# Kernel optimization log

Measured on AMD Instinct MI355X. Metric: run time of the kernel, lower is better.

Reference implementation:

```python
import jax, jax.numpy as jnp
import numpy as np

B = 64          # graphs per batch
MAX_NODES = 512 # nodes per graph
N = B * MAX_NODES
DEG = 16
E = N * DEG
F_IN = 12
H, D = 4, 32    # heads, per-head dim
HID = H * D     # 128
A = 512         # num_outputs (action space)
NEG_SLOPE = 0.2


def setup_inputs() -> dict:
    key = jax.random.key(0)
    ks = jax.random.split(key, 32)
    x = jax.random.normal(ks[0], (N, F_IN), dtype=jnp.float32)
    # edges confined within each graph's node block (as in the torch adjacency loop)
    src_l = jax.random.randint(ks[1], (B, MAX_NODES * DEG), 0, MAX_NODES, dtype=jnp.int32)
    dst_l = jax.random.randint(ks[2], (B, MAX_NODES * DEG), 0, MAX_NODES, dtype=jnp.int32)
    offs = (jnp.arange(B, dtype=jnp.int32) * MAX_NODES)[:, None]
    edge_src = (src_l + offs).reshape(-1)
    edge_dst = (dst_l + offs).reshape(-1)
    batch_idx = jnp.repeat(jnp.arange(B, dtype=jnp.int32), MAX_NODES)

    s = 0.1
    p = {}
    p["Wl0"] = s * jax.random.normal(ks[3], (F_IN, H, D), dtype=jnp.float32)
    p["Wr0"] = s * jax.random.normal(ks[4], (F_IN, H, D), dtype=jnp.float32)
    p["att0"] = s * jax.random.normal(ks[5], (H, D), dtype=jnp.float32)
    p["b0"] = jnp.zeros((HID,), dtype=jnp.float32)
    p["Wl"] = s * jax.random.normal(ks[6], (3, HID, H, D), dtype=jnp.float32)
    p["Wr"] = s * jax.random.normal(ks[7], (3, HID, H, D), dtype=jnp.float32)
    p["att"] = s * jax.random.normal(ks[8], (3, H, D), dtype=jnp.float32)
    p["b"] = jnp.zeros((3, HID), dtype=jnp.float32)
    p["qW1"] = s * jax.random.normal(ks[9], (2 * HID, HID), dtype=jnp.float32)
    p["qb1"] = jnp.zeros((HID,), dtype=jnp.float32)
    p["qW2"] = s * jax.random.normal(ks[10], (HID, A), dtype=jnp.float32)
    p["qb2"] = jnp.zeros((A,), dtype=jnp.float32)
    p["vW1"] = s * jax.random.normal(ks[11], (2 * HID, HID), dtype=jnp.float32)
    p["vb1"] = jnp.zeros((HID,), dtype=jnp.float32)
    p["vW2"] = s * jax.random.normal(ks[12], (HID, 1), dtype=jnp.float32)
    p["vb2"] = jnp.zeros((1,), dtype=jnp.float32)
    return dict(x=x, edge_src=edge_src, edge_dst=edge_dst, batch_idx=batch_idx, **p)


def _gatv2(x, src, dst, Wl, Wr, att, b):
    n = x.shape[0]
    xl = jnp.einsum('nf,fhd->nhd', x, Wl)  # source transform [N,H,D]
    xr = jnp.einsum('nf,fhd->nhd', x, Wr)  # target transform [N,H,D]
    xj = xl[src]                            # [E,H,D]
    e = jax.nn.leaky_relu(xj + xr[dst], NEG_SLOPE)
    s = jnp.einsum('ehd,hd->eh', e, att)    # [E,H]
    smax = jax.ops.segment_max(s, dst, num_segments=n)
    smax = jnp.where(jnp.isfinite(smax), smax, 0.0)
    a = jnp.exp(s - smax[dst])
    den = jax.ops.segment_sum(a, dst, num_segments=n)
    a = a / jnp.maximum(den[dst], 1e-16)
    out = jax.ops.segment_sum(a[:, :, None] * xj, dst, num_segments=n)  # [N,H,D]
    return out.reshape(n, H * D) + b


def reference(x, edge_src, edge_dst, batch_idx,
              Wl0, Wr0, att0, b0, Wl, Wr, att, b,
              qW1, qb1, qW2, qb2, vW1, vb1, vW2, vb2):
    h = jax.nn.relu(_gatv2(x, edge_src, edge_dst, Wl0, Wr0, att0, b0))
    for i in range(3):  # remaining num_layers-1 GATv2 layers (dropout off in eval)
        h = jax.nn.relu(_gatv2(h, edge_src, edge_dst, Wl[i], Wr[i], att[i], b[i]))
    nb = h.shape[0] // MAX_NODES
    gsum = jax.ops.segment_sum(h, batch_idx, num_segments=nb)
    cnt = jax.ops.segment_sum(jnp.ones((h.shape[0], 1), h.dtype), batch_idx, num_segments=nb)
    gmean = gsum / jnp.maximum(cnt, 1.0)
    gmax = jax.ops.segment_max(h, batch_idx, num_segments=nb)
    g = jnp.concatenate([gmean, gmax], axis=-1)  # [B, 2*HID]
    adv = jax.nn.relu(g @ qW1 + qb1) @ qW2 + qb2
    val = jax.nn.relu(g @ vW1 + vb1) @ vW2 + vb2
    q = val + (adv - adv.mean(axis=-1, keepdims=True))
    return q
```

## Files before the change

### kernel.cpp

```cpp
#include <hip/hip_runtime.h>
#include <hip/hip_bf16.h>

#define NN 32768
#define EE 524288
#define HID 128
#define BGRAPH 64
#define MAXN 512
#define AOUT 512
#define MAXDEG 64

typedef __attribute__((ext_vector_type(8))) short short8;
typedef __attribute__((ext_vector_type(4))) float f32x4;
typedef unsigned short ushort;
typedef unsigned int uint;

__device__ __forceinline__ ushort bf16_rn(float f) {
    uint u = __float_as_uint(f);
    u += 0x7FFF + ((u >> 16) & 1);
    return (ushort)(u >> 16);
}
__device__ __forceinline__ void bf16_split(float f, ushort& hi, ushort& lo) {
    hi = bf16_rn(f);
    float fh = __uint_as_float(((uint)hi) << 16);
    lo = bf16_rn(f - fh);
}

__device__ __forceinline__ float vsum4(f32x4 v) {
    return (v.x + v.y) + (v.z + v.w);
}

__global__ __launch_bounds__(256) void setup_kernel(
    const int* __restrict__ src, const int* __restrict__ dst,
    int* __restrict__ cursor, int* __restrict__ bucket,
    const float* __restrict__ Wl, const float* __restrict__ Wr,
    ushort* __restrict__ wt_hi, ushort* __restrict__ wt_lo) {
    int blk = blockIdx.x;
    if (blk < EE / 256) {
        int i = blk * 256 + threadIdx.x;
        int d = dst[i];
        int p = atomicAdd(&cursor[d], 1);
        if (p < MAXDEG) bucket[(size_t)d * MAXDEG + p] = src[i];
    } else {
        int idx = (blk - EE / 256) * 256 + threadIdx.x;
        if (idx >= 98304) return;
        int c = idx & 127;
        int k = (idx >> 7) & 127;
        int l = (idx >> 14) % 3;
        int lr = idx / 49152;
        float v = (lr ? Wr : Wl)[l * 16384 + k * 128 + c];
        ushort hi, lo;
        bf16_split(v, hi, lo);
        int ct = c >> 4, m = c & 15;
        int ks = k >> 5;
        int lane = (((k >> 3) & 3) << 4) | m;
        int j = k & 7;
        size_t o = ((size_t)(lr * 3 + l) * 32 + ct * 4 + ks) * 512 + lane * 8 + j;
        wt_hi[o] = hi;
        wt_lo[o] = lo;
    }
}

template<int KTOT, int KC>
__global__ __launch_bounds__(256) void transform3(
    const float* __restrict__ hin, const float* __restrict__ Wl,
    const float* __restrict__ Wr, float* __restrict__ xl, float* __restrict__ xr) {
    __shared__ float wb[KC][256];
    __shared__ float ha[KC][36];
    int b = blockIdx.x;
    int xcd = b & 7, slot = b >> 3;
    int graph = xcd + 8 * (slot >> 4);
    int chunk = slot & 15;
    int node0 = graph * 512 + chunk * 32;
    int t = threadIdx.x;
    int c32 = t & 31;
    int ng  = t >> 5;
    const float4* wl4g = (const float4*)Wl;
    const float4* wr4g = (const float4*)Wr;
    for (int idx = t; idx < KC * 64; idx += 256) {
        int k = idx >> 6, r = idx & 63;
        float4 v = (r < 32) ? wl4g[k * 32 + r] : wr4g[k * 32 + (r - 32)];
        ((float4*)&wb[k][0])[r] = v;
    }
    for (int idx = t; idx < 32 * KC; idx += 256) {
        int m = idx / KC, kk = idx - m * KC;
        ha[kk][m] = hin[(size_t)(node0 + m) * KTOT + kk];
    }
    __syncthreads();
    float4 accL[4], accR[4];
#pragma unroll
    for (int m = 0; m < 4; m++) {
        accL[m].x = accL[m].y = accL[m].z = accL[m].w = 0.f;
        accR[m].x = accR[m].y = accR[m].z = accR[m].w = 0.f;
    }
#pragma unroll
    for (int kk = 0; kk < KC; kk++) {
        float4 wl = ((const float4*)&wb[kk][0])[c32];
        float4 wr = ((const float4*)&wb[kk][128])[c32];
        float4 hv = *(const float4*)&ha[kk][ng * 4];
        accL[0].x = fmaf(hv.x, wl.x, accL[0].x); accL[0].y = fmaf(hv.x, wl.y, accL[0].y);
        accL[0].z = fmaf(hv.x, wl.z, accL[0].z); accL[0].w = fmaf(hv.x, wl.w, accL[0].w);
        accL[1].x = fmaf(hv.y, wl.x, accL[1].x); accL[1].y = fmaf(hv.y, wl.y, accL[1].y);
        accL[1].z = fmaf(hv.y, wl.z, accL[1].z); accL[1].w = fmaf(hv.y, wl.w, accL[1].w);
        accL[2].x = fmaf(hv.z, wl.x, accL[2].x); accL[2].y = fmaf(hv.z, wl.y, accL[2].y);
        accL[2].z = fmaf(hv.z, wl.z, accL[2].z); accL[2].w = fmaf(hv.z, wl.w, accL[2].w);
        accL[3].x = fmaf(hv.w, wl.x, accL[3].x); accL[3].y = fmaf(hv.w, wl.y, accL[3].y);
        accL[3].z = fmaf(hv.w, wl.z, accL[3].z); accL[3].w = fmaf(hv.w, wl.w, accL[3].w);
        accR[0].x = fmaf(hv.x, wr.x, accR[0].x); accR[0].y = fmaf(hv.x, wr.y, accR[0].y);
        accR[0].z = fmaf(hv.x, wr.z, accR[0].z); accR[0].w = fmaf(hv.x, wr.w, accR[0].w);
        accR[1].x = fmaf(hv.y, wr.x, accR[1].x); accR[1].y = fmaf(hv.y, wr.y, accR[1].y);
        accR[1].z = fmaf(hv.y, wr.z, accR[1].z); accR[1].w = fmaf(hv.y, wr.w, accR[1].w);
        accR[2].x = fmaf(hv.z, wr.x, accR[2].x); accR[2].y = fmaf(hv.z, wr.y, accR[2].y);
        accR[2].z = fmaf(hv.z, wr.z, accR[2].z); accR[2].w = fmaf(hv.z, wr.w, accR[2].w);
        accR[3].x = fmaf(hv.w, wr.x, accR[3].x); accR[3].y = fmaf(hv.w, wr.y, accR[3].y);
        accR[3].z = fmaf(hv.w, wr.z, accR[3].z); accR[3].w = fmaf(hv.w, wr.w, accR[3].w);
    }
    float4* xlo = (float4*)xl;
    float4* xro = (float4*)xr;
#pragma unroll
    for (int m = 0; m < 4; m++) {
        int n = node0 + ng * 4 + m;
        xlo[n * 32 + c32] = accL[m];
        xro[n * 32 + c32] = accR[m];
    }
}

__device__ __forceinline__ void gat_node_one(
    const f32x4* __restrict__ xl4, const int* __restrict__ brow,
    int nE, int n, f32x4 xr0, f32x4 xr1,
    int el4, int p16, f32x4 at0, f32x4 at1,
    f32x4& o0, f32x4& o1) {
    f32x4 a0 = {0.f, 0.f, 0.f, 0.f};
    f32x4 a1 = {0.f, 0.f, 0.f, 0.f};
    float den = 0.f;
    int nB = (nE + 3) >> 2;
    int e = el4;
    int s0i = (e < nE) ? brow[e] : n;
    const f32x4* r0 = xl4 + (size_t)s0i * 32 + p16 * 2;
    f32x4 cv0 = r0[0], cv1 = r0[1];
    for (int blk = 0; blk < nB; blk++) {
        f32x4 pv0, pv1;
        if (blk + 1 < nB) {
            int en = e + 4;
            int eni = en > (MAXDEG - 1) ? (MAXDEG - 1) : en;
            int sn = (en < nE) ? brow[eni] : n;
            const f32x4* rn = xl4 + (size_t)sn * 32 + p16 * 2;
            pv0 = rn[0]; pv1 = rn[1];
        }
        f32x4 u0 = cv0 + xr0;
        f32x4 u1 = cv1 + xr1;
        f32x4 l0 = __builtin_elementwise_max(u0, 0.2f * u0);
        f32x4 l1 = __builtin_elementwise_max(u1, 0.2f * u1);
        f32x4 tv = at0 * l0 + at1 * l1;
        float t = vsum4(tv);
        t += __shfl_xor(t, 1);
        t += __shfl_xor(t, 2);
        float a = (e < nE) ? __expf(t) : 0.f;
        den += a;
        a0 += a * cv0;
        a1 += a * cv1;
        if (blk + 1 < nB) { cv0 = pv0; cv1 = pv1; }
        e += 4;
    }
#define RED2(v) \
    v.x += __shfl_xor(v.x, 16); v.y += __shfl_xor(v.y, 16);                      \
    v.z += __shfl_xor(v.z, 16); v.w += __shfl_xor(v.w, 16);                      \
    v.x += __shfl_xor(v.x, 32); v.y += __shfl_xor(v.y, 32);                      \
    v.z += __shfl_xor(v.z, 32); v.w += __shfl_xor(v.w, 32);
    RED2(a0) RED2(a1)
#undef RED2
    den += __shfl_xor(den, 16);
    den += __shfl_xor(den, 32);
    float rden = 1.0f / fmaxf(den, 1e-16f);
    o0 = a0 * rden;
    o1 = a1 * rden;
}

__device__ __forceinline__ f32x4 relu_bias(f32x4 o, f32x4 bv) {
    f32x4 z = {0.f, 0.f, 0.f, 0.f};
    return __builtin_elementwise_max(o + bv, z);
}

__device__ __forceinline__ void store_h(f32x4 o0, f32x4 o1,
                                        ushort (*hh)[136], ushort (*hl)[136],
                                        int nl, int p16) {
    float f[8];
    f[0] = o0.x; f[1] = o0.y; f[2] = o0.z; f[3] = o0.w;
    f[4] = o1.x; f[5] = o1.y; f[6] = o1.z; f[7] = o1.w;
    ushort hi[8], lo[8];
#pragma unroll
    for (int i = 0; i < 8; i++) bf16_split(f[i], hi[i], lo[i]);
    uint4 ph, pl;
    ph.x = (uint)hi[0] | ((uint)hi[1] << 16);
    ph.y = (uint)hi[2] | ((uint)hi[3] << 16);
    ph.z = (uint)hi[4] | ((uint)hi[5] << 16);
    ph.w = (uint)hi[6] | ((uint)hi[7] << 16);
    pl.x = (uint)lo[0] | ((uint)lo[1] << 16);
    pl.y = (uint)lo[2] | ((uint)lo[3] << 16);
    pl.z = (uint)lo[4] | ((uint)lo[5] << 16);
    pl.w = (uint)lo[6] | ((uint)lo[7] << 16);
    *(uint4*)&hh[nl][p16 * 8] = ph;
    *(uint4*)&hl[nl][p16 * 8] = pl;
}

__global__ __launch_bounds__(256, 4) void fused_agg_mfma(
    const float* __restrict__ xl_in, const float* __restrict__ xr_in,
    const int* __restrict__ bucket, const int* __restrict__ cnt,
    const float* __restrict__ att, const float* __restrict__ bias,
    const ushort* __restrict__ wl_hi, const ushort* __restrict__ wl_lo,
    const ushort* __restrict__ wr_hi, const ushort* __restrict__ wr_lo,
    float* __restrict__ xl_out, float* __restrict__ xr_out) {
    __shared__ ushort hh[16][136];
    __shared__ ushort hl[16][136];
    int b = blockIdx.x;
    int xcd = b & 7, slot = b >> 3;
    int graph = xcd + 8 * (slot >> 5);
    int chunk = slot & 31;
    int node_base = graph * 512 + chunk * 16;
    int wid = threadIdx.x >> 6;
    int lane = threadIdx.x & 63;
    int el4 = (lane >> 4) & 3;
    int p16 = lane & 15;
    {
        const f32x4* xl4 = (const f32x4*)xl_in;
        const f32x4* xr4 = (const f32x4*)xr_in;
        const f32x4* att4 = (const f32x4*)att;
        const f32x4* bias4 = (const f32x4*)bias;
        f32x4 at0 = att4[p16 * 2];
        f32x4 at1 = att4[p16 * 2 + 1];
        f32x4 b0v = bias4[p16 * 2];
        f32x4 b1v = bias4[p16 * 2 + 1];
        int n0 = node_base + wid * 4;
        int nE[4];
        f32x4 xr0[4], xr1[4];
#pragma unroll
        for (int i = 0; i < 4; i++) {
            int n = n0 + i;
            int d = cnt[n];
            nE[i] = (d > MAXDEG) ? MAXDEG : d;
            xr0[i] = xr4[(size_t)n * 32 + p16 * 2];
            xr1[i] = xr4[(size_t)n * 32 + p16 * 2 + 1];
        }
#pragma unroll 1
        for (int i = 0; i < 4; i++) {
            int n = n0 + i;
            f32x4 o0, o1;
            gat_node_one(xl4, bucket + (size_t)n * MAXDEG, nE[i], n,
                         xr0[i], xr1[i], el4, p16, at0, at1, o0, o1);
            if (el4 == 0) {
                o0 = relu_bias(o0, b0v);
                o1 = relu_bias(o1, b1v);
                store_h(o0, o1, hh, hl, wid * 4 + i, p16);
            }
        }
    }
    __syncthreads();
    int m = lane & 15, quad = lane >> 4;
    f32x4 accL[2], accR[2];
#pragma unroll
    for (int c2 = 0; c2 < 2; c2++) {
        accL[c2] = (f32x4){0.f, 0.f, 0.f, 0.f};
        accR[c2] = (f32x4){0.f, 0.f, 0.f, 0.f};
    }
#pragma unroll
    for (int ks = 0; ks < 4; ks++) {
        short8 ah = *(const short8*)&hh[m][ks * 32 + quad * 8];
        short8 al = *(const short8*)&hl[m][ks * 32 + quad * 8];
#pragma unroll
        for (int c2 = 0; c2 < 2; c2++) {
            int ct = wid * 2 + c2;
            size_t wb = ((size_t)(ct * 4 + ks) * 64 + lane) * 8;
            short8 bhl = *(const short8*)(wl_hi + wb);
            short8 bll = *(const short8*)(wl_lo + wb);
            short8 bhr = *(const short8*)(wr_hi + wb);
            short8 blr = *(const short8*)(wr_lo + wb);
            accL[c2] = __builtin_amdgcn_mfma_f32_16x16x32_bf16(ah, bhl, accL[c2], 0, 0, 0);
            accL[c2] = __builtin_amdgcn_mfma_f32_16x16x32_bf16(ah, bll, accL[c2], 0, 0, 0);
            accL[c2] = __builtin_amdgcn_mfma_f32_16x16x32_bf16(al, bhl, accL[c2], 0, 0, 0);
            accR[c2] = __builtin_amdgcn_mfma_f32_16x16x32_bf16(ah, bhr, accR[c2], 0, 0, 0);
            accR[c2] = __builtin_amdgcn_mfma_f32_16x16x32_bf16(ah, blr, accR[c2], 0, 0, 0);
            accR[c2] = __builtin_amdgcn_mfma_f32_16x16x32_bf16(al, bhr, accR[c2], 0, 0, 0);
        }
    }
#pragma unroll
    for (int c2 = 0; c2 < 2; c2++) {
        int ct = wid * 2 + c2;
#pragma unroll
        for (int r = 0; r < 4; r++) {
            int node = node_base + quad * 4 + r;
            xl_out[(size_t)node * 128 + ct * 16 + m] = accL[c2][r];
            xr_out[(size_t)node * 128 + ct * 16 + m] = accR[c2][r];
        }
    }
}

__global__ __launch_bounds__(256, 4) void agg_pool(
    const float* __restrict__ xl_in, const float* __restrict__ xr_in,
    const int* __restrict__ bucket, const int* __restrict__ cnt,
    const float* __restrict__ att, const float* __restrict__ bias,
    float* __restrict__ psum, float* __restrict__ pmax) {
    __shared__ float sums[4][128];
    __shared__ float maxs[4][128];
    int b = blockIdx.x;
    int xcd = b & 7, slot = b >> 3;
    int graph = xcd + 8 * (slot >> 5);
    int chunk = slot & 31;
    int wid = threadIdx.x >> 6;
    int lane = threadIdx.x & 63;
    int el4 = (lane >> 4) & 3;
    int p16 = lane & 15;
    const f32x4* xl4 = (const f32x4*)xl_in;
    const f32x4* xr4 = (const f32x4*)xr_in;
    const f32x4* att4 = (const f32x4*)att;
    const f32x4* bias4 = (const f32x4*)bias;
    f32x4 at0 = att4[p16 * 2];
    f32x4 at1 = att4[p16 * 2 + 1];
    f32x4 b0v = bias4[p16 * 2];
    f32x4 b1v = bias4[p16 * 2 + 1];
    int node_base = graph * 512 + chunk * 16;
    int n0 = node_base + wid * 4;
    int nE[4];
    f32x4 xr0[4], xr1[4];
#pragma unroll
    for (int i = 0; i < 4; i++) {
        int n = n0 + i;
        int d = cnt[n];
        nE[i] = (d > MAXDEG) ? MAXDEG : d;
        xr0[i] = xr4[(size_t)n * 32 + p16 * 2];
        xr1[i] = xr4[(size_t)n * 32 + p16 * 2 + 1];
    }
    f32x4 s0 = {0.f, 0.f, 0.f, 0.f};
    f32x4 s1 = {0.f, 0.f, 0.f, 0.f};
    f32x4 m0 = {-1e30f, -1e30f, -1e30f, -1e30f};
    f32x4 m1 = {-1e30f, -1e30f, -1e30f, -1e30f};
#pragma unroll 1
    for (int i = 0; i < 4; i++) {
        int n = n0 + i;
        f32x4 o0, o1;
        gat_node_one(xl4, bucket + (size_t)n * MAXDEG, nE[i], n,
                     xr0[i], xr1[i], el4, p16, at0, at1, o0, o1);
        o0 = relu_bias(o0, b0v);
        o1 = relu_bias(o1, b1v);
        s0 += o0; s1 += o1;
        m0 = __builtin_elementwise_max(m0, o0);
        m1 = __builtin_elementwise_max(m1, o1);
    }
    if (el4 == 0) {
        *(f32x4*)&sums[wid][p16 * 8]     = s0;
        *(f32x4*)&sums[wid][p16 * 8 + 4] = s1;
        *(f32x4*)&maxs[wid][p16 * 8]     = m0;
        *(f32x4*)&maxs[wid][p16 * 8 + 4] = m1;
    }
    __syncthreads();
    int t = threadIdx.x;
    if (t < 128) {
        float s = 0.f, m = -1e30f;
#pragma unroll
        for (int ww = 0; ww < 4; ww++) {
            s += sums[ww][t];
            m = fmaxf(m, maxs[ww][t]);
        }
        psum[((size_t)graph * 32 + chunk) * 128 + t] = s;
        pmax[((size_t)graph * 32 + chunk) * 128 + t] = m;
    }
}

__global__ __launch_bounds__(512) void head_kernel(
    const float* __restrict__ psum, const float* __restrict__ pmax,
    const float* __restrict__ qW1, const float* __restrict__ qb1,
    const float* __restrict__ qW2, const float* __restrict__ qb2,
    const float* __restrict__ vW1, const float* __restrict__ vb1,
    const float* __restrict__ vW2, const float* __restrict__ vb2,
    float* __restrict__ qout) {
    __shared__ float gs[256];
    __shared__ float hq[128];
    __shared__ float hv[128];
    __shared__ float red[512];
    int b = blockIdx.x, t = threadIdx.x;
    if (t < 128) {
        float s = 0.f, m = -1e30f;
#pragma unroll 8
        for (int c = 0; c < 32; c++) {
            s += psum[((size_t)b * 32 + c) * 128 + t];
            m = fmaxf(m, pmax[((size_t)b * 32 + c) * 128 + t]);
        }
        gs[t] = s * (1.0f / 512.0f);
        gs[128 + t] = m;
    }
    __syncthreads();
    if (t < 128) {
        float acc = qb1[t];
        for (int k = 0; k < 256; k++) acc = fmaf(gs[k], qW1[k * 128 + t], acc);
        hq[t] = fmaxf(acc, 0.f);
    } else if (t < 256) {
        int tt = t - 128;
        float acc = vb1[tt];
        for (int k = 0; k < 256; k++) acc = fmaf(gs[k], vW1[k * 128 + tt], acc);
        hv[tt] = fmaxf(acc, 0.f);
    }
    __syncthreads();
    float adv = qb2[t];
    for (int k = 0; k < 128; k++) adv = fmaf(hq[k], qW2[k * 512 + t], adv);
    red[t] = (t < 128) ? hv[t] * vW2[t] : 0.f;
    __syncthreads();
    for (int off = 256; off > 0; off >>= 1) {
        if (t < off) red[t] += red[t + off];
        __syncthreads();
    }
    float val = red[0] + vb2[0];
    __syncthreads();
    red[t] = adv;
    __syncthreads();
    for (int off = 256; off > 0; off >>= 1) {
        if (t < off) red[t] += red[t + off];
        __syncthreads();
    }
    float mean_adv = red[0] * (1.0f / 512.0f);
    qout[b * 512 + t] = val + adv - mean_adv;
}

extern "C" void kernel_launch(void* const* d_in, const int* in_sizes, int n_in,
                              void* d_out, int out_size, void* d_ws, size_t ws_size,
                              hipStream_t stream) {
    const float* x        = (const float*)d_in[0];
    const int* edge_src   = (const int*)d_in[1];
    const int* edge_dst   = (const int*)d_in[2];
    const float* Wl0 = (const float*)d_in[4];
    const float* Wr0 = (const float*)d_in[5];
    const float* att0 = (const float*)d_in[6];
    const float* b0 = (const float*)d_in[7];
    const float* Wl = (const float*)d_in[8];
    const float* Wr = (const float*)d_in[9];
    const float* att = (const float*)d_in[10];
    const float* bb = (const float*)d_in[11];
    const float* qW1 = (const float*)d_in[12];
    const float* qb1 = (const float*)d_in[13];
    const float* qW2 = (const float*)d_in[14];
    const float* qb2 = (const float*)d_in[15];
    const float* vW1 = (const float*)d_in[16];
    const float* vb1 = (const float*)d_in[17];
    const float* vW2 = (const float*)d_in[18];
    const float* vb2 = (const float*)d_in[19];

    int* cursor  = (int*)d_ws;
    int* bucket  = cursor + NN;
    float* fbase = (float*)(bucket + (size_t)NN * MAXDEG);
    float* xlA   = fbase;
    float* xrA   = xlA + NN * 128;
    float* xlB   = xrA + NN * 128;
    float* xrB   = xlB + NN * 128;
    float* psum  = xrB + NN * 128;
    float* pmax  = psum + BGRAPH * 32 * 128;
    ushort* wthi = (ushort*)(pmax + BGRAPH * 32 * 128);
    ushort* wtlo = wthi + 2 * 3 * 16384;

    hipMemsetAsync(cursor, 0, NN * sizeof(int), stream);
    setup_kernel<<<EE / 256 + 384, 256, 0, stream>>>(edge_src, edge_dst, cursor, bucket,
                                                     Wl, Wr, wthi, wtlo);

    transform3<12, 12><<<NN / 32, 256, 0, stream>>>(x, Wl0, Wr0, xlA, xrA);

    fused_agg_mfma<<<NN / 16, 256, 0, stream>>>(xlA, xrA, bucket, cursor, att0, b0,
                                                wthi + 0 * 16384, wtlo + 0 * 16384,
                                                wthi + 3 * 16384, wtlo + 3 * 16384,
                                                xlB, xrB);
    fused_agg_mfma<<<NN / 16, 256, 0, stream>>>(xlB, xrB, bucket, cursor, att, bb,
                                                wthi + 1 * 16384, wtlo + 1 * 16384,
                                                wthi + 4 * 16384, wtlo + 4 * 16384,
                                                xlA, xrA);
    fused_agg_mfma<<<NN / 16, 256, 0, stream>>>(xlA, xrA, bucket, cursor,
                                                att + 128, bb + 128,
                                                wthi + 2 * 16384, wtlo + 2 * 16384,
                                                wthi + 5 * 16384, wtlo + 5 * 16384,
                                                xlB, xrB);
    agg_pool<<<NN / 16, 256, 0, stream>>>(xlB, xrB, bucket, cursor,
                                          att + 256, bb + 256, psum, pmax);
    head_kernel<<<BGRAPH, 512, 0, stream>>>(psum, pmax, qW1, qb1, qW2, qb2,
                                            vW1, vb1, vW2, vb2, (float*)d_out);
}
```

Baseline: 314.6 us.

## Stage per-graph source features in LDS and split edges by source half

```diff
diff --git a/kernel.cpp b/kernel.cpp
--- a/kernel.cpp
+++ b/kernel.cpp
@@ -24,22 +24,31 @@
     float fh = __uint_as_float(((uint)hi) << 16);
     lo = bf16_rn(f - fh);
 }
-
 __device__ __forceinline__ float vsum4(f32x4 v) {
     return (v.x + v.y) + (v.z + v.w);
 }
+__device__ __forceinline__ f32x4 relu_bias(f32x4 o, f32x4 bv) {
+    f32x4 z = {0.f, 0.f, 0.f, 0.f};
+    return __builtin_elementwise_max(o + bv, z);
+}
 
 __global__ __launch_bounds__(256) void setup_kernel(
     const int* __restrict__ src, const int* __restrict__ dst,
-    int* __restrict__ cursor, int* __restrict__ bucket,
+    int* __restrict__ curF, int* __restrict__ curU, int* __restrict__ bucket,
     const float* __restrict__ Wl, const float* __restrict__ Wr,
     ushort* __restrict__ wt_hi, ushort* __restrict__ wt_lo) {
     int blk = blockIdx.x;
     if (blk < EE / 256) {
         int i = blk * 256 + threadIdx.x;
         int d = dst[i];
-        int p = atomicAdd(&cursor[d], 1);
-        if (p < MAXDEG) bucket[(size_t)d * MAXDEG + p] = src[i];
+        int s = src[i];
+        if ((s & 256) == 0) {
+            int p = atomicAdd(&curF[d], 1);
+            if (p < MAXDEG) bucket[(size_t)d * MAXDEG + p] = s;
+        } else {
+            int q = atomicAdd(&curU[d], 1);
+            if (q < MAXDEG) bucket[(size_t)d * MAXDEG + (MAXDEG - 1 - q)] = s;
+        }
     } else {
         int idx = (blk - EE / 256) * 256 + threadIdx.x;
         if (idx >= 98304) return;
@@ -124,60 +133,79 @@
     }
 }
 
-__device__ __forceinline__ void gat_node_one(
-    const f32x4* __restrict__ xl4, const int* __restrict__ brow,
-    int nE, int n, f32x4 xr0, f32x4 xr1,
-    int el4, int p16, f32x4 at0, f32x4 at1,
+__device__ __forceinline__ void agg_phase(
+    float* xs, const f32x4* xl4, const f32x4* xr4,
+    const int* bucket, const int* curF, const int* curU,
+    int gbase, int n0, int tid, int el4, int p16,
+    f32x4 at0, f32x4 at1,
+    f32x4 a0[4], f32x4 a1[4], float den[4]) {
+#pragma unroll
+    for (int i = 0; i < 4; i++) {
+        a0[i] = (f32x4){0.f, 0.f, 0.f, 0.f};
+        a1[i] = (f32x4){0.f, 0.f, 0.f, 0.f};
+        den[i] = 0.f;
+    }
+#pragma unroll 1
+    for (int p = 0; p < 2; p++) {
+        if (p) __syncthreads();
+        for (int idx = tid; idx < 256 * 32; idx += 1024) {
+            int row = idx >> 5, c4 = idx & 31;
+            *(f32x4*)&xs[row * 132 + c4 * 4] =
+                xl4[(size_t)(gbase + p * 256 + row) * 32 + c4];
+        }
+        __syncthreads();
+#pragma unroll
+        for (int ni = 0; ni < 4; ni++) {
+            int n = n0 + ni;
+            int cF = curF[n]; cF = cF > MAXDEG ? MAXDEG : cF;
+            int cU = curU[n]; cU = cU > MAXDEG ? MAXDEG : cU;
+            int cntE = p ? cU : cF;
+            int lo   = p ? MAXDEG - cU : 0;
+            f32x4 xr0 = xr4[(size_t)n * 32 + p16 * 2];
+            f32x4 xr1 = xr4[(size_t)n * 32 + p16 * 2 + 1];
+            const int* brow = bucket + (size_t)n * MAXDEG;
+            int nBlk = (cntE + 3) >> 2;
+            for (int blk = 0; blk < nBlk; blk++) {
+                int er = blk * 4 + el4;
+                int valid = er < cntE;
+                int e = lo + er;
+                int s = valid ? brow[e] : 0;
+                int local = valid ? ((s & 511) - p * 256) : 0;
+                const f32x4* r = (const f32x4*)&xs[local * 132 + p16 * 8];
+                f32x4 v0 = r[0], v1 = r[1];
+                f32x4 u0 = v0 + xr0, u1 = v1 + xr1;
+                f32x4 l0 = __builtin_elementwise_max(u0, 0.2f * u0);
+                f32x4 l1 = __builtin_elementwise_max(u1, 0.2f * u1);
+                f32x4 tv = at0 * l0 + at1 * l1;
+                float t = vsum4(tv);
+                t += __shfl_xor(t, 1);
+                t += __shfl_xor(t, 2);
+                float a = valid ? __expf(t) : 0.f;
+                den[ni] += a;
+                a0[ni] += a * v0;
+                a1[ni] += a * v1;
+            }
+        }
+    }
+    __syncthreads();
+}
+
+__device__ __forceinline__ void node_reduce(
+    f32x4& A0, f32x4& A1, float& D, f32x4 b0v, f32x4 b1v,
     f32x4& o0, f32x4& o1) {
-    f32x4 a0 = {0.f, 0.f, 0.f, 0.f};
-    f32x4 a1 = {0.f, 0.f, 0.f, 0.f};
-    float den = 0.f;
-    int nB = (nE + 3) >> 2;
-    int e = el4;
-    int s0i = (e < nE) ? brow[e] : n;
-    const f32x4* r0 = xl4 + (size_t)s0i * 32 + p16 * 2;
-    f32x4 cv0 = r0[0], cv1 = r0[1];
-    for (int blk = 0; blk < nB; blk++) {
-        f32x4 pv0, pv1;
-        if (blk + 1 < nB) {
-            int en = e + 4;
-            int eni = en > (MAXDEG - 1) ? (MAXDEG - 1) : en;
-            int sn = (en < nE) ? brow[eni] : n;
-            const f32x4* rn = xl4 + (size_t)sn * 32 + p16 * 2;
-            pv0 = rn[0]; pv1 = rn[1];
-        }
-        f32x4 u0 = cv0 + xr0;
-        f32x4 u1 = cv1 + xr1;
-        f32x4 l0 = __builtin_elementwise_max(u0, 0.2f * u0);
-        f32x4 l1 = __builtin_elementwise_max(u1, 0.2f * u1);
-        f32x4 tv = at0 * l0 + at1 * l1;
-        float t = vsum4(tv);
-        t += __shfl_xor(t, 1);
-        t += __shfl_xor(t, 2);
-        float a = (e < nE) ? __expf(t) : 0.f;
-        den += a;
-        a0 += a * cv0;
-        a1 += a * cv1;
-        if (blk + 1 < nB) { cv0 = pv0; cv1 = pv1; }
-        e += 4;
-    }
-#define RED2(v) \
-    v.x += __shfl_xor(v.x, 16); v.y += __shfl_xor(v.y, 16);                      \
-    v.z += __shfl_xor(v.z, 16); v.w += __shfl_xor(v.w, 16);                      \
-    v.x += __shfl_xor(v.x, 32); v.y += __shfl_xor(v.y, 32);                      \
-    v.z += __shfl_xor(v.z, 32); v.w += __shfl_xor(v.w, 32);
-    RED2(a0) RED2(a1)
-#undef RED2
-    den += __shfl_xor(den, 16);
-    den += __shfl_xor(den, 32);
-    float rden = 1.0f / fmaxf(den, 1e-16f);
-    o0 = a0 * rden;
-    o1 = a1 * rden;
-}
-
-__device__ __forceinline__ f32x4 relu_bias(f32x4 o, f32x4 bv) {
-    f32x4 z = {0.f, 0.f, 0.f, 0.f};
-    return __builtin_elementwise_max(o + bv, z);
+    A0.x += __shfl_xor(A0.x, 16); A0.y += __shfl_xor(A0.y, 16);
+    A0.z += __shfl_xor(A0.z, 16); A0.w += __shfl_xor(A0.w, 16);
+    A1.x += __shfl_xor(A1.x, 16); A1.y += __shfl_xor(A1.y, 16);
+    A1.z += __shfl_xor(A1.z, 16); A1.w += __shfl_xor(A1.w, 16);
+    A0.x += __shfl_xor(A0.x, 32); A0.y += __shfl_xor(A0.y, 32);
+    A0.z += __shfl_xor(A0.z, 32); A0.w += __shfl_xor(A0.w, 32);
+    A1.x += __shfl_xor(A1.x, 32); A1.y += __shfl_xor(A1.y, 32);
+    A1.z += __shfl_xor(A1.z, 32); A1.w += __shfl_xor(A1.w, 32);
+    D += __shfl_xor(D, 16);
+    D += __shfl_xor(D, 32);
+    float rd = 1.0f / fmaxf(D, 1e-16f);
+    o0 = relu_bias(A0 * rd, b0v);
+    o1 = relu_bias(A1 * rd, b1v);
 }
 
 __device__ __forceinline__ void store_h(f32x4 o0, f32x4 o1,
@@ -202,110 +230,101 @@
     *(uint4*)&hl[nl][p16 * 8] = pl;
 }
 
-__global__ __launch_bounds__(256, 4) void fused_agg_mfma(
+__global__ __launch_bounds__(1024, 4) void fused_agg_mfma(
     const float* __restrict__ xl_in, const float* __restrict__ xr_in,
-    const int* __restrict__ bucket, const int* __restrict__ cnt,
+    const int* __restrict__ bucket, const int* __restrict__ curF,
+    const int* __restrict__ curU,
     const float* __restrict__ att, const float* __restrict__ bias,
     const ushort* __restrict__ wl_hi, const ushort* __restrict__ wl_lo,
     const ushort* __restrict__ wr_hi, const ushort* __restrict__ wr_lo,
     float* __restrict__ xl_out, float* __restrict__ xr_out) {
-    __shared__ ushort hh[16][136];
-    __shared__ ushort hl[16][136];
+    __shared__ float xs[256 * 132];
     int b = blockIdx.x;
     int xcd = b & 7, slot = b >> 3;
-    int graph = xcd + 8 * (slot >> 5);
-    int chunk = slot & 31;
-    int node_base = graph * 512 + chunk * 16;
-    int wid = threadIdx.x >> 6;
-    int lane = threadIdx.x & 63;
+    int graph = xcd + 8 * (slot >> 3);
+    int chunk = slot & 7;
+    int gbase = graph * 512;
+    int node_base = gbase + chunk * 64;
+    int tid = threadIdx.x;
+    int wid = tid >> 6;
+    int lane = tid & 63;
     int el4 = (lane >> 4) & 3;
     int p16 = lane & 15;
+    const f32x4* xl4 = (const f32x4*)xl_in;
+    const f32x4* xr4 = (const f32x4*)xr_in;
+    const f32x4* att4 = (const f32x4*)att;
+    f32x4 at0 = att4[p16 * 2];
+    f32x4 at1 = att4[p16 * 2 + 1];
+    int n0 = node_base + wid * 4;
+    f32x4 a0[4], a1[4];
+    float den[4];
+    agg_phase(xs, xl4, xr4, bucket, curF, curU, gbase, n0, tid, el4, p16,
+              at0, at1, a0, a1, den);
+    ushort (*hh)[136] = (ushort(*)[136])xs;
+    ushort (*hl)[136] = (ushort(*)[136])(xs + 4352);
     {
-        const f32x4* xl4 = (const f32x4*)xl_in;
-        const f32x4* xr4 = (const f32x4*)xr_in;
-        const f32x4* att4 = (const f32x4*)att;
         const f32x4* bias4 = (const f32x4*)bias;
-        f32x4 at0 = att4[p16 * 2];
-        f32x4 at1 = att4[p16 * 2 + 1];
         f32x4 b0v = bias4[p16 * 2];
         f32x4 b1v = bias4[p16 * 2 + 1];
-        int n0 = node_base + wid * 4;
-        int nE[4];
-        f32x4 xr0[4], xr1[4];
-#pragma unroll
-        for (int i = 0; i < 4; i++) {
-            int n = n0 + i;
-            int d = cnt[n];
-            nE[i] = (d > MAXDEG) ? MAXDEG : d;
-            xr0[i] = xr4[(size_t)n * 32 + p16 * 2];
-            xr1[i] = xr4[(size_t)n * 32 + p16 * 2 + 1];
-        }
-#pragma unroll 1
-        for (int i = 0; i < 4; i++) {
-            int n = n0 + i;
+#pragma unroll
+        for (int ni = 0; ni < 4; ni++) {
             f32x4 o0, o1;
-            gat_node_one(xl4, bucket + (size_t)n * MAXDEG, nE[i], n,
-                         xr0[i], xr1[i], el4, p16, at0, at1, o0, o1);
-            if (el4 == 0) {
-                o0 = relu_bias(o0, b0v);
-                o1 = relu_bias(o1, b1v);
-                store_h(o0, o1, hh, hl, wid * 4 + i, p16);
-            }
+            node_reduce(a0[ni], a1[ni], den[ni], b0v, b1v, o0, o1);
+            if (el4 == 0) store_h(o0, o1, hh, hl, wid * 4 + ni, p16);
         }
     }
     __syncthreads();
     int m = lane & 15, quad = lane >> 4;
-    f32x4 accL[2], accR[2];
-#pragma unroll
-    for (int c2 = 0; c2 < 2; c2++) {
-        accL[c2] = (f32x4){0.f, 0.f, 0.f, 0.f};
-        accR[c2] = (f32x4){0.f, 0.f, 0.f, 0.f};
-    }
-#pragma unroll
-    for (int ks = 0; ks < 4; ks++) {
-        short8 ah = *(const short8*)&hh[m][ks * 32 + quad * 8];
-        short8 al = *(const short8*)&hl[m][ks * 32 + quad * 8];
-#pragma unroll
-        for (int c2 = 0; c2 < 2; c2++) {
-            int ct = wid * 2 + c2;
+#pragma unroll
+    for (int pp = 0; pp < 2; pp++) {
+        int pi = wid * 2 + pp;
+        int rt = pi >> 3;
+        int ct = pi & 7;
+        f32x4 accL = {0.f, 0.f, 0.f, 0.f};
+        f32x4 accR = {0.f, 0.f, 0.f, 0.f};
+#pragma unroll
+        for (int ks = 0; ks < 4; ks++) {
+            short8 ah = *(const short8*)&hh[rt * 16 + m][ks * 32 + quad * 8];
+            short8 al = *(const short8*)&hl[rt * 16 + m][ks * 32 + quad * 8];
             size_t wb = ((size_t)(ct * 4 + ks) * 64 + lane) * 8;
             short8 bhl = *(const short8*)(wl_hi + wb);
             short8 bll = *(const short8*)(wl_lo + wb);
             short8 bhr = *(const short8*)(wr_hi + wb);
             short8 blr = *(const short8*)(wr_lo + wb);
-            accL[c2] = __builtin_amdgcn_mfma_f32_16x16x32_bf16(ah, bhl, accL[c2], 0, 0, 0);
-            accL[c2] = __builtin_amdgcn_mfma_f32_16x16x32_bf16(ah, bll, accL[c2], 0, 0, 0);
-            accL[c2] = __builtin_amdgcn_mfma_f32_16x16x32_bf16(al, bhl, accL[c2], 0, 0, 0);
-            accR[c2] = __builtin_amdgcn_mfma_f32_16x16x32_bf16(ah, bhr, accR[c2], 0, 0, 0);
-            accR[c2] = __builtin_amdgcn_mfma_f32_16x16x32_bf16(ah, blr, accR[c2], 0, 0, 0);
-            accR[c2] = __builtin_amdgcn_mfma_f32_16x16x32_bf16(al, bhr, accR[c2], 0, 0, 0);
-        }
-    }
-#pragma unroll
-    for (int c2 = 0; c2 < 2; c2++) {
-        int ct = wid * 2 + c2;
+            accL = __builtin_amdgcn_mfma_f32_16x16x32_bf16(ah, bhl, accL, 0, 0, 0);
+            accL = __builtin_amdgcn_mfma_f32_16x16x32_bf16(ah, bll, accL, 0, 0, 0);
+            accL = __builtin_amdgcn_mfma_f32_16x16x32_bf16(al, bhl, accL, 0, 0, 0);
+            accR = __builtin_amdgcn_mfma_f32_16x16x32_bf16(ah, bhr, accR, 0, 0, 0);
+            accR = __builtin_amdgcn_mfma_f32_16x16x32_bf16(ah, blr, accR, 0, 0, 0);
+            accR = __builtin_amdgcn_mfma_f32_16x16x32_bf16(al, bhr, accR, 0, 0, 0);
+        }
 #pragma unroll
         for (int r = 0; r < 4; r++) {
-            int node = node_base + quad * 4 + r;
-            xl_out[(size_t)node * 128 + ct * 16 + m] = accL[c2][r];
-            xr_out[(size_t)node * 128 + ct * 16 + m] = accR[c2][r];
-        }
-    }
-}
-
-__global__ __launch_bounds__(256, 4) void agg_pool(
+            int node = node_base + rt * 16 + quad * 4 + r;
+            xl_out[(size_t)node * 128 + ct * 16 + m] = accL[r];
+            xr_out[(size_t)node * 128 + ct * 16 + m] = accR[r];
+        }
+    }
+}
+
+__global__ __launch_bounds__(1024, 4) void agg_pool(
     const float* __restrict__ xl_in, const float* __restrict__ xr_in,
-    const int* __restrict__ bucket, const int* __restrict__ cnt,
+    const int* __restrict__ bucket, const int* __restrict__ curF,
+    const int* __restrict__ curU,
     const float* __restrict__ att, const float* __restrict__ bias,
     float* __restrict__ psum, float* __restrict__ pmax) {
-    __shared__ float sums[4][128];
-    __shared__ float maxs[4][128];
+    __shared__ float xs[256 * 132];
+    __shared__ float sums[16][128];
+    __shared__ float maxs[16][128];
     int b = blockIdx.x;
     int xcd = b & 7, slot = b >> 3;
-    int graph = xcd + 8 * (slot >> 5);
-    int chunk = slot & 31;
-    int wid = threadIdx.x >> 6;
-    int lane = threadIdx.x & 63;
+    int graph = xcd + 8 * (slot >> 3);
+    int chunk = slot & 7;
+    int gbase = graph * 512;
+    int node_base = gbase + chunk * 64;
+    int tid = threadIdx.x;
+    int wid = tid >> 6;
+    int lane = tid & 63;
     int el4 = (lane >> 4) & 3;
     int p16 = lane & 15;
     const f32x4* xl4 = (const f32x4*)xl_in;
@@ -316,30 +335,19 @@
     f32x4 at1 = att4[p16 * 2 + 1];
     f32x4 b0v = bias4[p16 * 2];
     f32x4 b1v = bias4[p16 * 2 + 1];
-    int node_base = graph * 512 + chunk * 16;
     int n0 = node_base + wid * 4;
-    int nE[4];
-    f32x4 xr0[4], xr1[4];
-#pragma unroll
-    for (int i = 0; i < 4; i++) {
-        int n = n0 + i;
-        int d = cnt[n];
-        nE[i] = (d > MAXDEG) ? MAXDEG : d;
-        xr0[i] = xr4[(size_t)n * 32 + p16 * 2];
-        xr1[i] = xr4[(size_t)n * 32 + p16 * 2 + 1];
-    }
+    f32x4 a0[4], a1[4];
+    float den[4];
+    agg_phase(xs, xl4, xr4, bucket, curF, curU, gbase, n0, tid, el4, p16,
+              at0, at1, a0, a1, den);
     f32x4 s0 = {0.f, 0.f, 0.f, 0.f};
     f32x4 s1 = {0.f, 0.f, 0.f, 0.f};
     f32x4 m0 = {-1e30f, -1e30f, -1e30f, -1e30f};
     f32x4 m1 = {-1e30f, -1e30f, -1e30f, -1e30f};
-#pragma unroll 1
-    for (int i = 0; i < 4; i++) {
-        int n = n0 + i;
+#pragma unroll
+    for (int ni = 0; ni < 4; ni++) {
         f32x4 o0, o1;
-        gat_node_one(xl4, bucket + (size_t)n * MAXDEG, nE[i], n,
-                     xr0[i], xr1[i], el4, p16, at0, at1, o0, o1);
-        o0 = relu_bias(o0, b0v);
-        o1 = relu_bias(o1, b1v);
+        node_reduce(a0[ni], a1[ni], den[ni], b0v, b1v, o0, o1);
         s0 += o0; s1 += o1;
         m0 = __builtin_elementwise_max(m0, o0);
         m1 = __builtin_elementwise_max(m1, o1);
@@ -351,16 +359,15 @@
         *(f32x4*)&maxs[wid][p16 * 8 + 4] = m1;
     }
     __syncthreads();
-    int t = threadIdx.x;
-    if (t < 128) {
+    if (tid < 128) {
         float s = 0.f, m = -1e30f;
 #pragma unroll
-        for (int ww = 0; ww < 4; ww++) {
-            s += sums[ww][t];
-            m = fmaxf(m, maxs[ww][t]);
-        }
-        psum[((size_t)graph * 32 + chunk) * 128 + t] = s;
-        pmax[((size_t)graph * 32 + chunk) * 128 + t] = m;
+        for (int ww = 0; ww < 16; ww++) {
+            s += sums[ww][tid];
+            m = fmaxf(m, maxs[ww][tid]);
+        }
+        psum[((size_t)graph * 8 + chunk) * 128 + tid] = s;
+        pmax[((size_t)graph * 8 + chunk) * 128 + tid] = m;
     }
 }
 
@@ -378,10 +385,10 @@
     int b = blockIdx.x, t = threadIdx.x;
     if (t < 128) {
         float s = 0.f, m = -1e30f;
-#pragma unroll 8
-        for (int c = 0; c < 32; c++) {
-            s += psum[((size_t)b * 32 + c) * 128 + t];
-            m = fmaxf(m, pmax[((size_t)b * 32 + c) * 128 + t]);
+#pragma unroll
+        for (int c = 0; c < 8; c++) {
+            s += psum[((size_t)b * 8 + c) * 128 + t];
+            m = fmaxf(m, pmax[((size_t)b * 8 + c) * 128 + t]);
         }
         gs[t] = s * (1.0f / 512.0f);
         gs[128 + t] = m;
@@ -441,8 +448,9 @@
     const float* vW2 = (const float*)d_in[18];
     const float* vb2 = (const float*)d_in[19];
 
-    int* cursor  = (int*)d_ws;
-    int* bucket  = cursor + NN;
+    int* curF    = (int*)d_ws;
+    int* curU    = curF + NN;
+    int* bucket  = curU + NN;
     float* fbase = (float*)(bucket + (size_t)NN * MAXDEG);
     float* xlA   = fbase;
     float* xrA   = xlA + NN * 128;
@@ -453,27 +461,30 @@
     ushort* wthi = (ushort*)(pmax + BGRAPH * 32 * 128);
     ushort* wtlo = wthi + 2 * 3 * 16384;
 
-    hipMemsetAsync(cursor, 0, NN * sizeof(int), stream);
-    setup_kernel<<<EE / 256 + 384, 256, 0, stream>>>(edge_src, edge_dst, cursor, bucket,
+    hipMemsetAsync(curF, 0, 2 * NN * sizeof(int), stream);
+    setup_kernel<<<EE / 256 + 384, 256, 0, stream>>>(edge_src, edge_dst,
+                                                     curF, curU, bucket,
                                                      Wl, Wr, wthi, wtlo);
 
     transform3<12, 12><<<NN / 32, 256, 0, stream>>>(x, Wl0, Wr0, xlA, xrA);
 
-    fused_agg_mfma<<<NN / 16, 256, 0, stream>>>(xlA, xrA, bucket, cursor, att0, b0,
-                                                wthi + 0 * 16384, wtlo + 0 * 16384,
-                                                wthi + 3 * 16384, wtlo + 3 * 16384,
-                                                xlB, xrB);
-    fused_agg_mfma<<<NN / 16, 256, 0, stream>>>(xlB, xrB, bucket, cursor, att, bb,
-                                                wthi + 1 * 16384, wtlo + 1 * 16384,
-                                                wthi + 4 * 16384, wtlo + 4 * 16384,
-                                                xlA, xrA);
-    fused_agg_mfma<<<NN / 16, 256, 0, stream>>>(xlA, xrA, bucket, cursor,
-                                                att + 128, bb + 128,
-                                                wthi + 2 * 16384, wtlo + 2 * 16384,
-                                                wthi + 5 * 16384, wtlo + 5 * 16384,
-                                                xlB, xrB);
-    agg_pool<<<NN / 16, 256, 0, stream>>>(xlB, xrB, bucket, cursor,
-                                          att + 256, bb + 256, psum, pmax);
+    fused_agg_mfma<<<NN / 64, 1024, 0, stream>>>(xlA, xrA, bucket, curF, curU,
+                                                 att0, b0,
+                                                 wthi + 0 * 16384, wtlo + 0 * 16384,
+                                                 wthi + 3 * 16384, wtlo + 3 * 16384,
+                                                 xlB, xrB);
+    fused_agg_mfma<<<NN / 64, 1024, 0, stream>>>(xlB, xrB, bucket, curF, curU,
+                                                 att, bb,
+                                                 wthi + 1 * 16384, wtlo + 1 * 16384,
+                                                 wthi + 4 * 16384, wtlo + 4 * 16384,
+                                                 xlA, xrA);
+    fused_agg_mfma<<<NN / 64, 1024, 0, stream>>>(xlA, xrA, bucket, curF, curU,
+                                                 att + 128, bb + 128,
+                                                 wthi + 2 * 16384, wtlo + 2 * 16384,
+                                                 wthi + 5 * 16384, wtlo + 5 * 16384,
+                                                 xlB, xrB);
+    agg_pool<<<NN / 64, 1024, 0, stream>>>(xlB, xrB, bucket, curF, curU,
+                                           att + 256, bb + 256, psum, pmax);
     head_kernel<<<BGRAPH, 512, 0, stream>>>(psum, pmax, qW1, qb1, qW2, qb2,
                                             vW1, vb1, vW2, vb2, (float*)d_out);
 }
```

Result: slower. 383.0 us (+21.7%).
